# Kernel optimization log

Measured on AMD Instinct MI355X. Metric: run time of the kernel, lower is better.

The kernel has to match this reference:

```python
import jax, jax.numpy as jnp
import numpy as np

B, SX, SL, D, H = 4, 4096, 256, 1024, 16
DH = D // H
LN_EPS = 1e-5
RMS_EPS = 1e-8


def layernorm(x, g, b):
    mu = jnp.mean(x, axis=-1, keepdims=True)
    var = jnp.mean(jnp.square(x - mu), axis=-1, keepdims=True)
    return (x - mu) * jax.lax.rsqrt(var + LN_EPS) * g + b


def rmsnorm(x, gamma):
    # torch: norm = ||x||_2 * dim^-0.5 ; x / clamp(norm, eps) * gamma
    norm = jnp.sqrt(jnp.sum(jnp.square(x), axis=-1, keepdims=True)) * (DH ** -0.5)
    return x / jnp.maximum(norm, RMS_EPS) * gamma


def setup_inputs() -> dict:
    key = jax.random.key(0)
    ks = jax.random.split(key, 6)
    s = 0.02
    return {
        "x": jax.random.normal(ks[0], (B, SX, D), jnp.float32),
        "latents": jax.random.normal(ks[1], (B, SL, D), jnp.float32),
        "mask_x": jnp.ones((B, SX), jnp.float32),
        "mask_latent": jnp.ones((B, SL), jnp.float32),
        "ln_x_g": jnp.ones((D,), jnp.float32),
        "ln_x_b": jnp.zeros((D,), jnp.float32),
        "ln_l_g": jnp.ones((D,), jnp.float32),
        "ln_l_b": jnp.zeros((D,), jnp.float32),
        "Wq": jax.random.normal(ks[2], (D, D), jnp.float32) * s,
        "Wkv": jax.random.normal(ks[3], (D, 2 * D), jnp.float32) * s,
        "qk_gamma": jnp.ones((DH,), jnp.float32),
        "Wo": jax.random.normal(ks[4], (D, D), jnp.float32) * s,
    }


def reference(x, latents, mask_x, mask_latent, ln_x_g, ln_x_b, ln_l_g, ln_l_b, Wq, Wkv, qk_gamma, Wo):
    xn = layernorm(x, ln_x_g, ln_x_b)                       # [B,SX,D]
    ln = layernorm(latents, ln_l_g, ln_l_b)                 # [B,SL,D]

    q = (ln @ Wq).reshape(B, SL, H, DH).transpose(0, 2, 1, 3)      # [B,H,SL,DH]
    kv_in = jnp.concatenate([xn, ln], axis=1)                      # [B,SX+SL,D]
    kv = kv_in @ Wkv
    Skv = SX + SL
    k = kv[..., :D].reshape(B, Skv, H, DH).transpose(0, 2, 1, 3)   # [B,H,Skv,DH]
    v = kv[..., D:].reshape(B, Skv, H, DH).transpose(0, 2, 1, 3)

    # NOTE: original code applies query_norm to BOTH q and k (faithful to source)
    q = rmsnorm(q, qk_gamma)
    k = rmsnorm(k, qk_gamma)

    scores = jnp.einsum("bhqd,bhkd->bhqk", q, k) / np.sqrt(DH)     # [B,H,SL,Skv]

    kv_mask = jnp.concatenate([mask_x, mask_latent], axis=1)       # [B,Skv]
    mask = kv_mask[:, None, :] * mask_latent[:, :, None]           # [B,SL,Skv]
    add_mask = (1.0 - mask)[:, None, :, :] * jnp.finfo(scores.dtype).min
    attn = jax.nn.softmax(scores + add_mask, axis=-1)

    y = jnp.einsum("bhqk,bhkd->bhqd", attn, v)                     # [B,H,SL,DH]
    y = y.transpose(0, 2, 1, 3).reshape(B, SL, D)
    return y @ Wo
```

## Files before the change

kernel.cpp:

```cpp
#include <hip/hip_runtime.h>

#define NB   4
#define SXX  4096
#define SLL  256
#define DD   1024
#define HH   16
#define DHH  64
#define SKV  4352
#define MKV  17408
#define NSPLIT 8

typedef __attribute__((ext_vector_type(8))) short bfrag;
typedef __attribute__((ext_vector_type(4))) float facc;

__device__ __forceinline__ unsigned short f2bf(float f){
  unsigned u = __builtin_bit_cast(unsigned, f);
  u = (u + 0x7fffu + ((u >> 16) & 1u)) >> 16;
  return (unsigned short)u;
}
__device__ __forceinline__ float bf2f(unsigned short h){
  unsigned u = ((unsigned)h) << 16;
  return __builtin_bit_cast(float, u);
}

#define GLOAD_LDS16(g, lds) __builtin_amdgcn_global_load_lds( \
    (const __attribute__((address_space(1))) unsigned int*)(const void*)(g), \
    (__attribute__((address_space(3))) unsigned int*)(void*)(lds), 16, 0, 0)

__global__ void wtrans3(const float* __restrict__ Wq, const float* __restrict__ Wkv,
                        const float* __restrict__ Wo, unsigned short* __restrict__ wqt,
                        unsigned short* __restrict__ wkvt, unsigned short* __restrict__ wot){
  __shared__ float t[32][33];
  int z = blockIdx.z;
  const float* in; unsigned short* out; int N;
  if (z == 0){ in = Wq;  out = wqt;  N = DD;   }
  else if (z == 1){ in = Wkv; out = wkvt; N = 2*DD; }
  else { in = Wo;  out = wot;  N = DD;   }
  int n0 = blockIdx.x * 32, k0 = blockIdx.y * 32;
  if (n0 >= N) return;
  int tx = threadIdx.x, ty = threadIdx.y;
  #pragma unroll
  for (int i = 0; i < 4; i++)
    t[ty + 8*i][tx] = in[(size_t)(k0 + ty + 8*i) * N + n0 + tx];
  __syncthreads();
  #pragma unroll
  for (int i = 0; i < 4; i++)
    out[(size_t)(n0 + ty + 8*i) * DD + k0 + tx] = f2bf(t[tx][ty + 8*i]);
}

__global__ void lnorm(const float* __restrict__ src, const float* __restrict__ g,
                      const float* __restrict__ bt, unsigned short* __restrict__ kvin,
                      unsigned short* __restrict__ dst2, int seq, int off){
  int row = blockIdx.x;
  int b = row / seq, s = row - b*seq;
  int t = threadIdx.x;
  const float4* rp = (const float4*)(src + (size_t)row * DD);
  float4 v = rp[t];
  float sum = v.x + v.y + v.z + v.w;
  float sq  = v.x*v.x + v.y*v.y + v.z*v.z + v.w*v.w;
  #pragma unroll
  for (int o = 32; o > 0; o >>= 1){ sum += __shfl_down(sum, o); sq += __shfl_down(sq, o); }
  __shared__ float ls[8];
  int w = t >> 6, l = t & 63;
  if (l == 0){ ls[w] = sum; ls[4 + w] = sq; }
  __syncthreads();
  sum = ls[0] + ls[1] + ls[2] + ls[3];
  sq  = ls[4] + ls[5] + ls[6] + ls[7];
  float mu  = sum * (1.f/DD);
  float var = sq * (1.f/DD) - mu*mu;
  float rs  = rsqrtf(var + 1e-5f);
  float4 gv = ((const float4*)g)[t];
  float4 bv = ((const float4*)bt)[t];
  ushort4 o4;
  o4.x = f2bf((v.x - mu)*rs*gv.x + bv.x);
  o4.y = f2bf((v.y - mu)*rs*gv.y + bv.y);
  o4.z = f2bf((v.z - mu)*rs*gv.z + bv.z);
  o4.w = f2bf((v.w - mu)*rs*gv.w + bv.w);
  *(ushort4*)(kvin + (size_t)(b*SKV + off + s) * DD + t*4) = o4;
  if (dst2) *(ushort4*)(dst2 + (size_t)row * DD + t*4) = o4;
}

__global__ __launch_bounds__(256) void gemm64(const unsigned short* __restrict__ A,
    const unsigned short* __restrict__ Bt, int M, int N, int K, float* __restrict__ outF){
  __shared__ unsigned short lA[64][72];
  __shared__ unsigned short lB[64][72];
  int n0 = blockIdx.x * 64, m0 = blockIdx.y * 64;
  int t = threadIdx.x, w = t >> 6, l = t & 63;
  int wr = (w >> 1) * 32, wc = (w & 1) * 32;
  int lr = l & 15, kq = (l >> 4) * 8;
  facc acc00 = (facc)0.f, acc01 = (facc)0.f, acc10 = (facc)0.f, acc11 = (facc)0.f;
  for (int k0 = 0; k0 < K; k0 += 64){
    #pragma unroll
    for (int cc = 0; cc < 2; cc++){
      int ch = t + cc*256;
      int row = ch >> 3, cg = (ch & 7) * 8;
      *(bfrag*)&lA[row][cg] = *(const bfrag*)&A[(size_t)(m0 + row) * K + k0 + cg];
      *(bfrag*)&lB[row][cg] = *(const bfrag*)&Bt[(size_t)(n0 + row) * K + k0 + cg];
    }
    __syncthreads();
    #pragma unroll
    for (int ks = 0; ks < 2; ks++){
      bfrag a0 = *(const bfrag*)&lA[wr + lr][ks*32 + kq];
      bfrag a1 = *(const bfrag*)&lA[wr + 16 + lr][ks*32 + kq];
      bfrag b0 = *(const bfrag*)&lB[wc + lr][ks*32 + kq];
      bfrag b1 = *(const bfrag*)&lB[wc + 16 + lr][ks*32 + kq];
      acc00 = __builtin_amdgcn_mfma_f32_16x16x32_bf16(a0, b0, acc00, 0, 0, 0);
      acc01 = __builtin_amdgcn_mfma_f32_16x16x32_bf16(a0, b1, acc01, 0, 0, 0);
      acc10 = __builtin_amdgcn_mfma_f32_16x16x32_bf16(a1, b0, acc10, 0, 0, 0);
      acc11 = __builtin_amdgcn_mfma_f32_16x16x32_bf16(a1, b1, acc11, 0, 0, 0);
    }
    __syncthreads();
  }
  int rl = (l >> 4) * 4, cl = l & 15;
  facc accs[2][2] = {{acc00, acc01},{acc10, acc11}};
  #pragma unroll
  for (int mt = 0; mt < 2; mt++)
  #pragma unroll
  for (int nt = 0; nt < 2; nt++)
  #pragma unroll
  for (int j = 0; j < 4; j++){
    int r = m0 + wr + mt*16 + rl + j;
    int c = n0 + wc + nt*16 + cl;
    outF[(size_t)r * N + c] = accs[mt][nt][j];
  }
}

__global__ __launch_bounds__(256) void gemm_q(const unsigned short* __restrict__ A,
    const unsigned short* __restrict__ Bt, const float* __restrict__ gamma,
    unsigned short* __restrict__ qn){
  __shared__ char smemb[18432];
  unsigned short* lA = (unsigned short*)smemb;
  unsigned short* lB = lA + 64*72;
  float* Cf = (float*)smemb;
  int h = blockIdx.x, n0 = h * 64, m0 = blockIdx.y * 64;
  int t = threadIdx.x, w = t >> 6, l = t & 63;
  int wr = (w >> 1) * 32, wc = (w & 1) * 32;
  int lr = l & 15, kq = (l >> 4) * 8;
  facc acc00 = (facc)0.f, acc01 = (facc)0.f, acc10 = (facc)0.f, acc11 = (facc)0.f;
  for (int k0 = 0; k0 < 1024; k0 += 64){
    #pragma unroll
    for (int cc = 0; cc < 2; cc++){
      int ch = t + cc*256;
      int row = ch >> 3, cg = (ch & 7) * 8;
      *(bfrag*)&lA[row*72 + cg] = *(const bfrag*)&A[(size_t)(m0 + row) * 1024 + k0 + cg];
      *(bfrag*)&lB[row*72 + cg] = *(const bfrag*)&Bt[(size_t)(n0 + row) * 1024 + k0 + cg];
    }
    __syncthreads();
    #pragma unroll
    for (int ks = 0; ks < 2; ks++){
      bfrag a0 = *(const bfrag*)&lA[(wr + lr)*72 + ks*32 + kq];
      bfrag a1 = *(const bfrag*)&lA[(wr + 16 + lr)*72 + ks*32 + kq];
      bfrag b0 = *(const bfrag*)&lB[(wc + lr)*72 + ks*32 + kq];
      bfrag b1 = *(const bfrag*)&lB[(wc + 16 + lr)*72 + ks*32 + kq];
      acc00 = __builtin_amdgcn_mfma_f32_16x16x32_bf16(a0, b0, acc00, 0, 0, 0);
      acc01 = __builtin_amdgcn_mfma_f32_16x16x32_bf16(a0, b1, acc01, 0, 0, 0);
      acc10 = __builtin_amdgcn_mfma_f32_16x16x32_bf16(a1, b0, acc10, 0, 0, 0);
      acc11 = __builtin_amdgcn_mfma_f32_16x16x32_bf16(a1, b1, acc11, 0, 0, 0);
    }
    __syncthreads();
  }
  int rl = (l >> 4) * 4, cl = l & 15;
  facc accs[2][2] = {{acc00, acc01},{acc10, acc11}};
  #pragma unroll
  for (int mt = 0; mt < 2; mt++)
  #pragma unroll
  for (int nt = 0; nt < 2; nt++)
  #pragma unroll
  for (int j = 0; j < 4; j++)
    Cf[(wr + mt*16 + rl + j)*66 + wc + nt*16 + cl] = accs[mt][nt][j];
  __syncthreads();
  if (t < 64){
    const float* src = &Cf[t*66];
    float ss = 0.f;
    #pragma unroll
    for (int d = 0; d < 64; d++){ float a = src[d]; ss = fmaf(a, a, ss); }
    float rv = 0.125f / fmaxf(sqrtf(ss) * 0.125f, 1e-8f);
    int r = m0 + t, b = r >> 8, sl = r & 255;
    unsigned short* dst = &qn[((size_t)(b*HH + h)*SLL + sl)*DHH];
    #pragma unroll
    for (int i = 0; i < 8; i++){
      ushort4 p; float g;
      g = gamma[i*8+0]; p.x = f2bf(src[i*8+0]*g*g*rv);
      g = gamma[i*8+1]; p.y = f2bf(src[i*8+1]*g*g*rv);
      g = gamma[i*8+2]; p.z = f2bf(src[i*8+2]*g*g*rv);
      g = gamma[i*8+3]; p.w = f2bf(src[i*8+3]*g*g*rv);
      ushort4 q;
      g = gamma[i*8+4]; q.x = f2bf(src[i*8+4]*g*g*rv);
      g = gamma[i*8+5]; q.y = f2bf(src[i*8+5]*g*g*rv);
      g = gamma[i*8+6]; q.z = f2bf(src[i*8+6]*g*g*rv);
      g = gamma[i*8+7]; q.w = f2bf(src[i*8+7]*g*g*rv);
      *(ushort4*)&dst[i*8]     = p;
      *(ushort4*)&dst[i*8 + 4] = q;
    }
  }
}

__global__ __launch_bounds__(512, 2) void gemm_kv(const unsigned short* __restrict__ A,
    const unsigned short* __restrict__ Bt,
    const float* __restrict__ mask_x, const float* __restrict__ mask_lat,
    unsigned short* __restrict__ outK, unsigned short* __restrict__ outV,
    float* __restrict__ rkm){
  __shared__ alignas(16) unsigned short lds[3 * 24576];
  int bid = blockIdx.x;
  int wg = (bid & 7) * 136 + (bid >> 3);
  int m0 = (wg >> 4) * 256, n0 = (wg & 15) * 128;
  int t = threadIdx.x, w = t >> 6, l = t & 63;
  int wm = w >> 1, wn = w & 1;
  int lr = l & 15, q2 = l >> 4;
  int r8 = l >> 3, u = l & 7;
  int swz = (u ^ (r8 & 7)) * 8;
  const unsigned short* Ag = A  + (size_t)(m0 + w*8 + r8) * 1024 + swz;
  const unsigned short* Bg = Bt + (size_t)(n0 + w*8 + r8) * 1024 + swz;

  facc acc[4][4];
  #pragma unroll
  for (int mt = 0; mt < 4; mt++)
  #pragma unroll
  for (int nt = 0; nt < 4; nt++) acc[mt][nt] = (facc)0.f;

#define SBAR __builtin_amdgcn_sched_barrier(0)
#define KV_BARRIER do { SBAR; __builtin_amdgcn_s_barrier(); SBAR; } while(0)
#define KV_STA(j, i) GLOAD_LDS16(Ag + (size_t)(i)*65536 + (j)*64, \
    &lds[((j) % 3)*24576 + (i)*4096 + w*512])
#define KV_STB(j, i) GLOAD_LDS16(Bg + (size_t)(i)*65536 + (j)*64, \
    &lds[((j) % 3)*24576 + 16384 + (i)*4096 + w*512])
#define KV_LDF(va, vb, j, ks) { \
    const unsigned short* pA = &lds[((j) % 3)*24576 + (wm*64 + lr)*64 + (((ks)*4 + q2) ^ (lr & 7))*8]; \
    const unsigned short* pB = &lds[((j) % 3)*24576 + 16384 + (wn*64 + lr)*64 + (((ks)*4 + q2) ^ (lr & 7))*8]; \
    va[0] = *(const bfrag*)(pA);        va[1] = *(const bfrag*)(pA + 1024); \
    va[2] = *(const bfrag*)(pA + 2048); va[3] = *(const bfrag*)(pA + 3072); \
    vb[0] = *(const bfrag*)(pB);        vb[1] = *(const bfrag*)(pB + 1024); \
    vb[2] = *(const bfrag*)(pB + 2048); vb[3] = *(const bfrag*)(pB + 3072); }
#define KV_MFMA(va, vb) do { \
    __builtin_amdgcn_s_setprio(1); \
    _Pragma("unroll") \
    for (int mt = 0; mt < 4; mt++){ \
      _Pragma("unroll") \
      for (int nt = 0; nt < 4; nt++) \
        acc[mt][nt] = __builtin_amdgcn_mfma_f32_16x16x32_bf16(va[mt], vb[nt], acc[mt][nt], 0, 0, 0); } \
    __builtin_amdgcn_s_setprio(0); } while(0)

  KV_STA(0,0); KV_STA(0,1); KV_STA(0,2); KV_STA(0,3); KV_STB(0,0); KV_STB(0,1);
  KV_STA(1,0); KV_STA(1,1); KV_STA(1,2); KV_STA(1,3); KV_STB(1,0); KV_STB(1,1);
  __asm__ volatile("s_waitcnt vmcnt(6)" ::: "memory");
  KV_BARRIER;

  bfrag av[4], bv[4];
  #pragma unroll
  for (int j = 0; j < 16; j++){
    KV_LDF(av, bv, j, 0);
    if (j < 14){ KV_STA(j+2, 0); KV_STA(j+2, 1); KV_STB(j+2, 0); }
    KV_MFMA(av, bv);
    KV_LDF(av, bv, j, 1);
    if (j < 14){ KV_STA(j+2, 2); KV_STA(j+2, 3); KV_STB(j+2, 1); }
    KV_MFMA(av, bv);
    if (j < 14)       { __asm__ volatile("s_waitcnt vmcnt(6)" ::: "memory"); }
    else if (j == 14) { __asm__ volatile("s_waitcnt vmcnt(0)" ::: "memory"); }
    KV_BARRIER;
  }
#undef KV_STA
#undef KV_STB
#undef KV_LDF
#undef KV_MFMA

  int b = m0 / SKV, s0 = m0 - b*SKV;
  if (n0 < DD){
    #pragma unroll
    for (int mt = 0; mt < 4; mt++)
    #pragma unroll
    for (int nt = 0; nt < 4; nt++)
    #pragma unroll
    for (int j = 0; j < 4; j++)
      lds[(wm*64 + mt*16 + q2*4 + j)*136 + wn*64 + nt*16 + lr] = f2bf(acc[mt][nt][j]);
    __syncthreads();
    int s = t >> 1, hf = t & 1;
    int srow = s0 + s;
    float cm = (srow < SXX) ? mask_x[b*SXX + srow] : mask_lat[b*SLL + srow - SXX];
    const unsigned short* src = &lds[s*136 + hf*64];
    uint4 wv[8];
    #pragma unroll
    for (int i = 0; i < 8; i++) wv[i] = *(const uint4*)&src[i*8];
    float ss0 = 0.f, ss1 = 0.f;
    #pragma unroll
    for (int i = 0; i < 8; i++){
      const unsigned short* pp = (const unsigned short*)&wv[i];
      #pragma unroll
      for (int e = 0; e < 4; e++){
        float a = bf2f(pp[e]);     ss0 = fmaf(a, a, ss0);
        float c = bf2f(pp[e + 4]); ss1 = fmaf(c, c, ss1);
      }
    }
    float rv = 1.f / fmaxf(sqrtf(ss0 + ss1) * 0.125f, 1e-8f);
    int h = (n0 >> 6) + hf;
    unsigned short* dst = &outK[((size_t)(b*HH + h)*SKV + srow)*DHH];
    #pragma unroll
    for (int i = 0; i < 8; i++)
      *(uint4*)&dst[i*8] = wv[i];
    rkm[((size_t)(b*HH + h))*SKV + srow] = (cm != 0.f) ? rv : -1.f;
  } else {
    #pragma unroll
    for (int mt = 0; mt < 4; mt++)
    #pragma unroll
    for (int nt = 0; nt < 4; nt++){
      ushort4 p;
      p.x = f2bf(acc[mt][nt][0]); p.y = f2bf(acc[mt][nt][1]);
      p.z = f2bf(acc[mt][nt][2]); p.w = f2bf(acc[mt][nt][3]);
      *(ushort4*)&lds[(wn*64 + nt*16 + lr)*264 + wm*64 + mt*16 + q2*4] = p;
    }
    __syncthreads();
    int c = t >> 2, sq = t & 3;
    int hh = ((n0 - DD) >> 6) + (c >> 6), d = c & 63;
    const unsigned short* src = &lds[c*264 + sq*64];
    unsigned short* dst = &outV[((size_t)(b*HH + hh)*DHH + d)*SKV + s0 + sq*64];
    #pragma unroll
    for (int i = 0; i < 8; i++)
      *(uint4*)&dst[i*8] = *(const uint4*)&src[i*8];
  }
}

__global__ __launch_bounds__(256) void attn(const unsigned short* __restrict__ qn,
    const unsigned short* __restrict__ kbuf, const unsigned short* __restrict__ vT,
    const float* __restrict__ rkm, const float* __restrict__ mask_lat,
    float* __restrict__ Opart, float* __restrict__ lpart){
  int qt = blockIdx.x, bh = blockIdx.y, split = blockIdx.z;
  int b = bh >> 4;
  __shared__ unsigned short lP[4][2][16][68];
  int t = threadIdx.x, w = t >> 6, l = t & 63;
  int lr = l & 15, q2 = l >> 4, kq = q2 * 8;
  int q0 = qt * 128;
  bfrag aq0[2], aq1[2];
  float rm[2][4];
  #pragma unroll
  for (int tt = 0; tt < 2; tt++){
    const unsigned short* qbase = qn + ((size_t)bh * SLL + q0 + tt*64 + w*16 + lr) * DHH;
    aq0[tt] = *(const bfrag*)&qbase[kq];
    aq1[tt] = *(const bfrag*)&qbase[32 + kq];
    #pragma unroll
    for (int j = 0; j < 4; j++) rm[tt][j] = mask_lat[b*SLL + q0 + tt*64 + w*16 + q2*4 + j];
  }
  facc O[2][4];
  #pragma unroll
  for (int tt = 0; tt < 2; tt++)
  #pragma unroll
  for (int nt = 0; nt < 4; nt++) O[tt][nt] = (facc)0.f;
  float lsum[2][4];
  #pragma unroll
  for (int tt = 0; tt < 2; tt++)
  #pragma unroll
  for (int j = 0; j < 4; j++) lsum[tt][j] = 0.f;

  int t0 = (split * 68) / NSPLIT, t1 = ((split + 1) * 68) / NSPLIT;
  for (int kt = t0; kt < t1; kt++){
    int key0 = kt * 64;
    const unsigned short* kb = kbuf + ((size_t)bh * SKV + key0) * DHH;
    bfrag bk0[4], bk1[4]; float rk[4];
    #pragma unroll
    for (int nt = 0; nt < 4; nt++){
      bk0[nt] = *(const bfrag*)&kb[(nt*16 + lr)*DHH + kq];
      bk1[nt] = *(const bfrag*)&kb[(nt*16 + lr)*DHH + 32 + kq];
      rk[nt]  = rkm[(size_t)bh*SKV + key0 + nt*16 + lr];
    }
    facc S[2][4];
    #pragma unroll
    for (int tt = 0; tt < 2; tt++)
    #pragma unroll
    for (int nt = 0; nt < 4; nt++){
      S[tt][nt] = (facc)0.f;
      S[tt][nt] = __builtin_amdgcn_mfma_f32_16x16x32_bf16(aq0[tt], bk0[nt], S[tt][nt], 0, 0, 0);
      S[tt][nt] = __builtin_amdgcn_mfma_f32_16x16x32_bf16(aq1[tt], bk1[nt], S[tt][nt], 0, 0, 0);
    }
    const unsigned short* vb = vT + (size_t)bh * DHH * SKV + key0;
    bfrag bv0[4], bv1[4];
    #pragma unroll
    for (int nt = 0; nt < 4; nt++){
      bv0[nt] = *(const bfrag*)&vb[(size_t)(nt*16 + lr)*SKV + kq];
      bv1[nt] = *(const bfrag*)&vb[(size_t)(nt*16 + lr)*SKV + 32 + kq];
    }
    #pragma unroll
    for (int tt = 0; tt < 2; tt++){
      #pragma unroll
      for (int j = 0; j < 4; j++){
        float rs_ = 0.f;
        #pragma unroll
        for (int nt = 0; nt < 4; nt++){
          float x = S[tt][nt][j] * rk[nt];
          float sv = (rk[nt] >= 0.f && rm[tt][j] != 0.f) ? x : -3.0e38f;
          float p = __expf(sv - 8.0f);
          rs_ += p;
          lP[w][tt][q2*4 + j][nt*16 + lr] = f2bf(p);
        }
        lsum[tt][j] += rs_;
      }
    }
    __asm__ volatile("s_waitcnt lgkmcnt(0)" ::: "memory");
    bfrag ap0[2], ap1[2];
    #pragma unroll
    for (int tt = 0; tt < 2; tt++){
      ap0[tt] = *(const bfrag*)&lP[w][tt][lr][kq];
      ap1[tt] = *(const bfrag*)&lP[w][tt][lr][32 + kq];
    }
    #pragma unroll
    for (int nt = 0; nt < 4; nt++){
      #pragma unroll
      for (int tt = 0; tt < 2; tt++){
        O[tt][nt] = __builtin_amdgcn_mfma_f32_16x16x32_bf16(ap0[tt], bv0[nt], O[tt][nt], 0, 0, 0);
        O[tt][nt] = __builtin_amdgcn_mfma_f32_16x16x32_bf16(ap1[tt], bv1[nt], O[tt][nt], 0, 0, 0);
      }
    }
  }
  #pragma unroll
  for (int tt = 0; tt < 2; tt++)
  #pragma unroll
  for (int j = 0; j < 4; j++){
    float L = lsum[tt][j];
    L += __shfl_xor(L, 1); L += __shfl_xor(L, 2);
    L += __shfl_xor(L, 4); L += __shfl_xor(L, 8);
    int srow = q0 + tt*64 + w*16 + q2*4 + j;
    size_t obase = (((size_t)split*64 + bh)*SLL + srow)*DHH;
    #pragma unroll
    for (int nt = 0; nt < 4; nt++)
      Opart[obase + nt*16 + lr] = O[tt][nt][j];
    if (lr == 0)
      lpart[((size_t)split*64 + bh)*SLL + srow] = L;
  }
}

__global__ __launch_bounds__(256) void attn_combine(const float* __restrict__ Opart,
    const float* __restrict__ lpart, unsigned short* __restrict__ ybuf){
  int t = threadIdx.x, w = t >> 6, l = t & 63;
  int idx = blockIdx.x * 4 + w;
  int bh = idx >> 8, srow = idx & 255;
  int b = bh >> 4, h = bh & 15;
  float L = 0.f, acc = 0.f;
  #pragma unroll
  for (int s = 0; s < NSPLIT; s++){
    L   += lpart[((size_t)s*64 + bh)*SLL + srow];
    acc += Opart[(((size_t)s*64 + bh)*SLL + srow)*DHH + l];
  }
  ybuf[((size_t)b*SLL + srow)*DD + h*DHH + l] = f2bf(acc / L);
}

extern "C" void kernel_launch(void* const* d_in, const int* in_sizes, int n_in,
                              void* d_out, int out_size, void* d_ws, size_t ws_size,
                              hipStream_t stream) {
  const float* x        = (const float*)d_in[0];
  const float* latents  = (const float*)d_in[1];
  const float* mask_x   = (const float*)d_in[2];
  const float* mask_lat = (const float*)d_in[3];
  const float* ln_x_g   = (const float*)d_in[4];
  const float* ln_x_b   = (const float*)d_in[5];
  const float* ln_l_g   = (const float*)d_in[6];
  const float* ln_l_b   = (const float*)d_in[7];
  const float* Wq       = (const float*)d_in[8];
  const float* Wkv      = (const float*)d_in[9];
  const float* qk_gamma = (const float*)d_in[10];
  const float* Wo       = (const float*)d_in[11];
  float* out = (float*)d_out;

  char* wsb = (char*)d_ws;
  unsigned short* kvin  = (unsigned short*)(wsb + 0);
  unsigned short* lnlat = (unsigned short*)(wsb + 35651584);
  unsigned short* wqt   = (unsigned short*)(wsb + 37748736);
  unsigned short* wkvt  = (unsigned short*)(wsb + 39845888);
  unsigned short* wot   = (unsigned short*)(wsb + 44040192);
  unsigned short* qnb   = (unsigned short*)(wsb + 50331648);
  unsigned short* kbuf  = (unsigned short*)(wsb + 52428800);
  unsigned short* vT    = (unsigned short*)(wsb + 88080384);
  float*          rkm   = (float*)(wsb + 123731968);
  unsigned short* ybuf  = (unsigned short*)(wsb + 124846080);
  float*          Opart = (float*)(wsb + 0);
  float*          lpart = (float*)(wsb + 35651584);

  wtrans3<<<dim3(64, 32, 3), dim3(32, 8), 0, stream>>>(Wq, Wkv, Wo, wqt, wkvt, wot);

  lnorm<<<NB*SXX, 256, 0, stream>>>(x,       ln_x_g, ln_x_b, kvin, nullptr, SXX, 0);
  lnorm<<<NB*SLL, 256, 0, stream>>>(latents, ln_l_g, ln_l_b, kvin, lnlat,   SLL, SXX);

  gemm_q<<<dim3(16, 16), 256, 0, stream>>>(lnlat, wqt, qk_gamma, qnb);
  gemm_kv<<<dim3(1088), 512, 0, stream>>>(kvin, wkvt, mask_x, mask_lat, kbuf, vT, rkm);

  attn<<<dim3(SLL/128, NB*HH, NSPLIT), 256, 0, stream>>>(qnb, kbuf, vT, rkm, mask_lat, Opart, lpart);
  attn_combine<<<(NB*HH*SLL)/4, 256, 0, stream>>>(Opart, lpart, ybuf);

  gemm64<<<dim3(DD/64, (NB*SLL)/64), 256, 0, stream>>>(ybuf, wot, NB*SLL, DD, DD, out);
}
```

Before: 369.8 us.

## Load B operand fragments directly from global into registers in KV GEMM

The B tile of the K/V projection GEMM is no longer staged through LDS. Each wave reads its B fragments straight from global memory into double-buffered registers one k-step ahead, while A keeps the 3-stage LDS pipeline. This shrinks LDS use, which may allow higher occupancy, and removes the LDS write and read traffic for B. In exchange each wave pair loads the same B data redundantly, uses more VGPRs, and must absorb global load latency within a single iteration.

New measurement: 476.8 us. 1.29x slower.

```diff
diff --git a/kernel.cpp b/kernel.cpp
--- a/kernel.cpp
+++ b/kernel.cpp
@@ -200,7 +200,7 @@
     const float* __restrict__ mask_x, const float* __restrict__ mask_lat,
     unsigned short* __restrict__ outK, unsigned short* __restrict__ outV,
     float* __restrict__ rkm){
-  __shared__ alignas(16) unsigned short lds[3 * 24576];
+  __shared__ alignas(16) unsigned short lds[3 * 16384];
   int bid = blockIdx.x;
   int wg = (bid & 7) * 136 + (bid >> 3);
   int m0 = (wg >> 4) * 256, n0 = (wg & 15) * 128;
@@ -209,8 +209,8 @@
   int lr = l & 15, q2 = l >> 4;
   int r8 = l >> 3, u = l & 7;
   int swz = (u ^ (r8 & 7)) * 8;
-  const unsigned short* Ag = A  + (size_t)(m0 + w*8 + r8) * 1024 + swz;
-  const unsigned short* Bg = Bt + (size_t)(n0 + w*8 + r8) * 1024 + swz;
+  const unsigned short* Ag = A + (size_t)(m0 + w*8 + r8) * 1024 + swz;
+  const unsigned short* Bg2 = Bt + (size_t)(n0 + wn*64 + lr) * 1024 + q2*8;
 
   facc acc[4][4];
   #pragma unroll
@@ -221,16 +221,17 @@
 #define SBAR __builtin_amdgcn_sched_barrier(0)
 #define KV_BARRIER do { SBAR; __builtin_amdgcn_s_barrier(); SBAR; } while(0)
 #define KV_STA(j, i) GLOAD_LDS16(Ag + (size_t)(i)*65536 + (j)*64, \
-    &lds[((j) % 3)*24576 + (i)*4096 + w*512])
-#define KV_STB(j, i) GLOAD_LDS16(Bg + (size_t)(i)*65536 + (j)*64, \
-    &lds[((j) % 3)*24576 + 16384 + (i)*4096 + w*512])
-#define KV_LDF(va, vb, j, ks) { \
-    const unsigned short* pA = &lds[((j) % 3)*24576 + (wm*64 + lr)*64 + (((ks)*4 + q2) ^ (lr & 7))*8]; \
-    const unsigned short* pB = &lds[((j) % 3)*24576 + 16384 + (wn*64 + lr)*64 + (((ks)*4 + q2) ^ (lr & 7))*8]; \
+    &lds[((j) % 3)*16384 + (i)*4096 + w*512])
+#define KV_LDB(dst, j) { \
+    const unsigned short* pB = Bg2 + (size_t)(j)*64; \
+    dst[0][0] = *(const bfrag*)(pB);              dst[0][1] = *(const bfrag*)(pB + 16384); \
+    dst[0][2] = *(const bfrag*)(pB + 32768);      dst[0][3] = *(const bfrag*)(pB + 49152); \
+    dst[1][0] = *(const bfrag*)(pB + 32);         dst[1][1] = *(const bfrag*)(pB + 16384 + 32); \
+    dst[1][2] = *(const bfrag*)(pB + 32768 + 32); dst[1][3] = *(const bfrag*)(pB + 49152 + 32); }
+#define KV_LDFA(va, j, ks) { \
+    const unsigned short* pA = &lds[((j) % 3)*16384 + (wm*64 + lr)*64 + (((ks)*4 + q2) ^ (lr & 7))*8]; \
     va[0] = *(const bfrag*)(pA);        va[1] = *(const bfrag*)(pA + 1024); \
-    va[2] = *(const bfrag*)(pA + 2048); va[3] = *(const bfrag*)(pA + 3072); \
-    vb[0] = *(const bfrag*)(pB);        vb[1] = *(const bfrag*)(pB + 1024); \
-    vb[2] = *(const bfrag*)(pB + 2048); vb[3] = *(const bfrag*)(pB + 3072); }
+    va[2] = *(const bfrag*)(pA + 2048); va[3] = *(const bfrag*)(pA + 3072); }
 #define KV_MFMA(va, vb) do { \
     __builtin_amdgcn_s_setprio(1); \
     _Pragma("unroll") \
@@ -240,27 +241,30 @@
         acc[mt][nt] = __builtin_amdgcn_mfma_f32_16x16x32_bf16(va[mt], vb[nt], acc[mt][nt], 0, 0, 0); } \
     __builtin_amdgcn_s_setprio(0); } while(0)
 
-  KV_STA(0,0); KV_STA(0,1); KV_STA(0,2); KV_STA(0,3); KV_STB(0,0); KV_STB(0,1);
-  KV_STA(1,0); KV_STA(1,1); KV_STA(1,2); KV_STA(1,3); KV_STB(1,0); KV_STB(1,1);
-  __asm__ volatile("s_waitcnt vmcnt(6)" ::: "memory");
+  bfrag bb[2][2][4];
+  bfrag av0[4], av1[4];
+
+  KV_STA(0,0); KV_STA(0,1); KV_STA(0,2); KV_STA(0,3);
+  KV_STA(1,0); KV_STA(1,1); KV_STA(1,2); KV_STA(1,3);
+  KV_LDB(bb[0], 0);
+  __asm__ volatile("s_waitcnt vmcnt(12)" ::: "memory");
   KV_BARRIER;
 
-  bfrag av[4], bv[4];
   #pragma unroll
   for (int j = 0; j < 16; j++){
-    KV_LDF(av, bv, j, 0);
-    if (j < 14){ KV_STA(j+2, 0); KV_STA(j+2, 1); KV_STB(j+2, 0); }
-    KV_MFMA(av, bv);
-    KV_LDF(av, bv, j, 1);
-    if (j < 14){ KV_STA(j+2, 2); KV_STA(j+2, 3); KV_STB(j+2, 1); }
-    KV_MFMA(av, bv);
-    if (j < 14)       { __asm__ volatile("s_waitcnt vmcnt(6)" ::: "memory"); }
-    else if (j == 14) { __asm__ volatile("s_waitcnt vmcnt(0)" ::: "memory"); }
+    if (j < 15) KV_LDB(bb[(j+1)&1], j+1);
+    if (j < 14){ KV_STA(j+2,0); KV_STA(j+2,1); KV_STA(j+2,2); KV_STA(j+2,3); }
+    KV_LDFA(av0, j, 0);
+    KV_LDFA(av1, j, 1);
+    KV_MFMA(av0, bb[j&1][0]);
+    KV_MFMA(av1, bb[j&1][1]);
+    if (j < 14)       { __asm__ volatile("s_waitcnt vmcnt(12)" ::: "memory"); }
+    else if (j == 14) { __asm__ volatile("s_waitcnt vmcnt(8)" ::: "memory"); }
     KV_BARRIER;
   }
 #undef KV_STA
-#undef KV_STB
-#undef KV_LDF
+#undef KV_LDB
+#undef KV_LDFA
 #undef KV_MFMA
 
   int b = m0 / SKV, s0 = m0 - b*SKV;
```
